# Kernel optimization log

Hardware: AMD Instinct MI355X
Metric: run time of the kernel (lower is better)

## Reference

```python
import jax, jax.numpy as jnp
import numpy as np

N = 20000      # CG beads
F = 78         # n_atom_basis (forced by reshape(-1,78) + Linear(n_atom_basis,39))
NRBF = 20
CUTOFF = 21.0
L = 3          # num_conv
DEG = 16
EH = N * DEG // 2
EPS = 1e-15


def silu(x):
    return x * jax.nn.sigmoid(x)


def setup_inputs() -> dict:
    key = jax.random.key(0)
    ks = jax.random.split(key, 22)
    cg_xyz = jax.random.normal(ks[0], (N, 3), jnp.float32) * 10.0
    half = jax.random.randint(ks[1], (EH, 2), 0, N)
    # symmetric (already-directed) edge list -> make_directed is a no-op
    CG_nbr_list = jnp.concatenate([half, half[:, ::-1]], axis=0)
    H = jax.random.normal(ks[2], (N, F), jnp.float32)
    mapping = jax.random.randint(ks[3], (N,), 0, N)  # unused by forward
    s = 0.05
    p = lambda k, shape: jax.random.normal(k, shape, jnp.float32) * s
    return {
        'cg_xyz': cg_xyz, 'CG_nbr_list': CG_nbr_list, 'mapping': mapping, 'H': H,
        # message blocks (stacked over L layers): inv_dense (F->F->4F) + dist_embed dense (NRBF->4F)
        'msg_w1': p(ks[4], (L, F, F)),   'msg_b1': jnp.zeros((L, F)),
        'msg_w2': p(ks[5], (L, F, 4 * F)), 'msg_b2': jnp.zeros((L, 4 * F)),
        'rbf_w':  p(ks[6], (L, NRBF, 4 * F)), 'rbf_b': jnp.zeros((L, 4 * F)),
        # update blocks: U, V linear maps (no bias) + s_dense (2F->F->3F)
        'upd_wu': p(ks[7], (L, F, F)), 'upd_wv': p(ks[8], (L, F, F)),
        'upd_w1': p(ks[9], (L, 2 * F, F)), 'upd_b1': jnp.zeros((L, F)),
        'upd_w2': p(ks[10], (L, F, 3 * F)), 'upd_b2': jnp.zeros((L, 3 * F)),
        # final dense head: ReLU -> Linear(78,39) -> ReLU -> Linear(39,39)
        'dense_w1': p(ks[11], (F, 39)), 'dense_b1': jnp.zeros((39,)),
        'dense_w2': p(ks[12], (39, 39)), 'dense_b2': jnp.zeros((39,)),
    }


def reference(cg_xyz, CG_nbr_list, mapping, H,
              msg_w1, msg_b1, msg_w2, msg_b2, rbf_w, rbf_b,
              upd_wu, upd_wv, upd_w1, upd_b1, upd_w2, upd_b2,
              dense_w1, dense_b1, dense_w2, dense_b2):
    n_nodes = H.shape[0]
    i_idx = CG_nbr_list[:, 0]
    j_idx = CG_nbr_list[:, 1]
    # edge geometry (shared across layers)
    r_ij = cg_xyz[j_idx] - cg_xyz[i_idx]                      # (E,3)
    dist = jnp.sqrt((r_ij ** 2 + EPS).sum(-1))                # (E,)
    unit = r_ij / dist[:, None]
    n = jnp.arange(1, NRBF + 1, dtype=cg_xyz.dtype)
    rbf = jnp.sin(n * jnp.pi * dist[:, None] / CUTOFF) / dist[:, None]   # (E,NRBF)
    env = jnp.where(dist < CUTOFF, 0.5 * (jnp.cos(jnp.pi * dist / CUTOFF) + 1.0), 0.0)

    V = jnp.zeros((n_nodes, H.shape[1], 3), H.dtype)          # (N,F,3)
    for l in range(L):
        # ---- EquiMessageCross ----
        phi = silu(H @ msg_w1[l] + msg_b1[l]) @ msg_w2[l] + msg_b2[l]     # (N,4F)
        w_s = (rbf @ rbf_w[l] + rbf_b[l]) * env[:, None]                  # (E,4F)
        inv = phi[j_idx] * w_s                                            # (E,4F)
        s0, s1, s2, s3 = jnp.split(inv, 4, axis=-1)                       # each (E,F)
        vj = V[j_idx]                                                     # (E,F,3)
        vi = V[i_idx]
        dv = (s2[..., None] * unit[:, None, :]
              + s1[..., None] * vj
              + s3[..., None] * jnp.cross(vi, vj, axis=-1))               # (E,F,3)
        H = H + jax.ops.segment_sum(s0, i_idx, num_segments=n_nodes)
        V = V + jax.ops.segment_sum(dv, i_idx, num_segments=n_nodes)
        # ---- UpdateBlock (PaiNN) ----
        u_v = jnp.einsum('nfc,fg->ngc', V, upd_wu[l])
        v_v = jnp.einsum('nfc,fg->ngc', V, upd_wv[l])
        v_norm = jnp.sqrt((v_v ** 2).sum(-1) + EPS)                       # (N,F)
        a = silu(jnp.concatenate([H, v_norm], -1) @ upd_w1[l] + upd_b1[l]) @ upd_w2[l] + upd_b2[l]
        a_vv, a_sv, a_ss = jnp.split(a, 3, axis=-1)
        H = H + a_sv * (u_v * v_v).sum(-1) + a_ss
        V = V + a_vv[..., None] * u_v

    Vs = V.sum(-1).reshape(-1, 78)                                        # (N,78)
    out = jax.nn.relu(Vs)
    out = jax.nn.relu(out @ dense_w1 + dense_b1) @ dense_w2 + dense_b2    # (N,39)
    return H, out.reshape(-1, 13, 3)
```

## Files before the change

### kernel.cpp

```cpp
#include <hip/hip_runtime.h>
#include <hip/hip_bf16.h>
#include <cmath>

#define N_NODES 20000
#define FF 78
#define F3 234
#define F4 312
#define NRBF 20
#define CUTOFF 21.0f
#define NL 3
#define PI_F 3.14159265358979323846f
#define EPS_F 1e-15f
#define REC_STRIDE 24
#define CHUNK 64
#define UV_RN 16

__global__ void k_init(const float* __restrict__ Hin, float* __restrict__ Hcur,
                       int* __restrict__ counts, int* __restrict__ cursor)
{
    int idx = blockIdx.x * blockDim.x + threadIdx.x;
    int stride = gridDim.x * blockDim.x;
    for (int i = idx; i < N_NODES * FF; i += stride) {
        Hcur[i] = Hin[i];
        if (i < N_NODES) { counts[i] = 0; cursor[i] = 0; }
    }
}

__global__ void k_geo(const float* __restrict__ xyz, const int* __restrict__ nbr,
                      float4* __restrict__ geo, int* __restrict__ counts, int E)
{
    int e = blockIdx.x * blockDim.x + threadIdx.x;
    if (e >= E) return;
    int i = nbr[2 * e], j = nbr[2 * e + 1];
    float rx = xyz[3 * j]     - xyz[3 * i];
    float ry = xyz[3 * j + 1] - xyz[3 * i + 1];
    float rz = xyz[3 * j + 2] - xyz[3 * i + 2];
    float d = sqrtf(rx * rx + ry * ry + rz * rz + 3.0f * EPS_F);
    geo[e] = make_float4(rx / d, ry / d, rz / d, d);
    if (d < CUTOFF) atomicAdd(&counts[i], 1);
}

__global__ __launch_bounds__(1024)
void k_scan(const int* __restrict__ counts, int* __restrict__ row_start, int n)
{
    __shared__ int s[1024];
    const int t = threadIdx.x;
    constexpr int PER = 20;
    const int base = t * PER;
    int loc[PER];
    int sum = 0;
    #pragma unroll
    for (int q = 0; q < PER; ++q) {
        int idx = base + q;
        int v = (idx < n) ? counts[idx] : 0;
        loc[q] = sum;
        sum += v;
    }
    s[t] = sum;
    __syncthreads();
    for (int off = 1; off < 1024; off <<= 1) {
        int add = (t >= off) ? s[t - off] : 0;
        __syncthreads();
        s[t] += add;
        __syncthreads();
    }
    const int excl = (t > 0) ? s[t - 1] : 0;
    #pragma unroll
    for (int q = 0; q < PER; ++q) {
        int idx = base + q;
        if (idx <= n) row_start[idx] = excl + loc[q];
    }
}

__global__ void k_fill(const float4* __restrict__ geo, const int* __restrict__ nbr,
                       const int* __restrict__ row_start, int* __restrict__ cursor,
                       float* __restrict__ rec, int* __restrict__ jl, int E)
{
    int e = blockIdx.x * blockDim.x + threadIdx.x;
    if (e >= E) return;
    float4 g = geo[e];
    if (g.w < CUTOFF) {
        int i = nbr[2 * e];
        int pos = row_start[i] + atomicAdd(&cursor[i], 1);
        float d = g.w;
        float theta = PI_F * d / CUTOFF;
        float s1, c1;
        sincosf(theta, &s1, &c1);
        float env = 0.5f * (c1 + 1.0f);
        float envd = env / d;
        float* r = rec + (size_t)pos * REC_STRIDE;
        float twoc = 2.f * c1;
        float skm = 0.f, sk = s1;
        r[0] = envd * sk;
        #pragma unroll
        for (int k = 1; k < NRBF; ++k) {
            float sk1 = twoc * sk - skm;
            r[k] = envd * sk1;
            skm = sk; sk = sk1;
        }
        r[20] = env;
        r[21] = g.x; r[22] = g.y; r[23] = g.z;
        jl[pos] = nbr[2 * e + 1];
    }
}

template<int K1T, int K2T, int NC2, int CS2, int BF16OUT>
__global__ void k_mlp2(const float* __restrict__ X1, const float* __restrict__ X2,
                       const float* __restrict__ w1, const float* __restrict__ b1,
                       const float* __restrict__ w2, const float* __restrict__ b2,
                       void* __restrict__ Yv, int nrows)
{
    constexpr int R = 32;
    constexpr int K = K1T + K2T;
    __shared__ float sX[K * R];
    __shared__ float s2[78 * 33];
    const int r0 = blockIdx.x * R;
    const int tid = threadIdx.y * 78 + threadIdx.x;
    for (int idx = tid; idx < R * K; idx += 312) {
        int r = idx / K, k = idx - r * K;
        int row = r0 + r;
        float v = 0.f;
        if (row < nrows) {
            if constexpr (K2T == 0) v = X1[(size_t)row * K1T + k];
            else v = (k < K1T) ? X1[(size_t)row * K1T + k] : X2[(size_t)row * K2T + (k - K1T)];
        }
        sX[k * R + r] = v;
    }
    __syncthreads();
    const int rg = threadIdx.y * 8;
    {
        const int c = threadIdx.x;
        float acc[8];
        #pragma unroll
        for (int q = 0; q < 8; ++q) acc[q] = 0.f;
        for (int k = 0; k < K; ++k) {
            const float w = w1[k * 78 + c];
            #pragma unroll
            for (int q = 0; q < 8; ++q) acc[q] = fmaf(w, sX[k * R + rg + q], acc[q]);
        }
        const float bb = b1[c];
        #pragma unroll
        for (int q = 0; q < 8; ++q) {
            float y = acc[q] + bb;
            y = y / (1.f + expf(-y));
            s2[c * 33 + rg + q] = y;
        }
    }
    __syncthreads();
    {
        const int c0 = threadIdx.x * CS2;
        float acc[8][CS2];
        #pragma unroll
        for (int q = 0; q < 8; ++q)
            #pragma unroll
            for (int cc = 0; cc < CS2; ++cc) acc[q][cc] = 0.f;
        for (int k = 0; k < 78; ++k) {
            float xv[8];
            #pragma unroll
            for (int q = 0; q < 8; ++q) xv[q] = s2[k * 33 + rg + q];
            float wv[CS2];
            #pragma unroll
            for (int cc = 0; cc < CS2; ++cc) wv[cc] = w2[(size_t)k * NC2 + c0 + cc];
            #pragma unroll
            for (int q = 0; q < 8; ++q)
                #pragma unroll
                for (int cc = 0; cc < CS2; ++cc) acc[q][cc] = fmaf(xv[q], wv[cc], acc[q][cc]);
        }
        #pragma unroll
        for (int q = 0; q < 8; ++q) {
            int row = r0 + rg + q;
            if (row < nrows) {
                if constexpr (BF16OUT && CS2 == 4) {
                    union { __hip_bfloat16 hh[4]; uint2 u; } pk;
                    #pragma unroll
                    for (int cc = 0; cc < 4; ++cc)
                        pk.hh[cc] = __float2bfloat16(acc[q][cc] + b2[c0 + cc]);
                    *(uint2*)&((__hip_bfloat16*)Yv)[(size_t)row * NC2 + c0] = pk.u;
                } else {
                    #pragma unroll
                    for (int cc = 0; cc < CS2; ++cc)
                        ((float*)Yv)[(size_t)row * NC2 + c0 + cc] = acc[q][cc] + b2[c0 + cc];
                }
            }
        }
    }
}

__global__ __launch_bounds__(312)
void k_updmlp_apply(const float* __restrict__ H, const float* __restrict__ vnorm,
                    const float* __restrict__ w1, const float* __restrict__ b1,
                    const float* __restrict__ w2, const float* __restrict__ b2,
                    const float* __restrict__ u_v, const float* __restrict__ v_v,
                    float* __restrict__ V, __hip_bfloat16* __restrict__ Vbf,
                    float* __restrict__ Hout)
{
    constexpr int R = 32;
    __shared__ float sX[156 * R];
    __shared__ float s2[78 * 33];
    const int r0 = blockIdx.x * R;
    const int tid = threadIdx.y * 78 + threadIdx.x;
    for (int idx = tid; idx < R * 156; idx += 312) {
        int r = idx / 156, k = idx - r * 156;
        int row = r0 + r;
        sX[k * R + r] = (k < 78) ? H[(size_t)row * FF + k]
                                 : vnorm[(size_t)row * FF + (k - 78)];
    }
    __syncthreads();
    const int rg = threadIdx.y * 8;
    const int c = threadIdx.x;
    {
        float acc[8];
        #pragma unroll
        for (int q = 0; q < 8; ++q) acc[q] = 0.f;
        for (int k = 0; k < 156; ++k) {
            const float w = w1[k * 78 + c];
            #pragma unroll
            for (int q = 0; q < 8; ++q) acc[q] = fmaf(w, sX[k * R + rg + q], acc[q]);
        }
        const float bb = b1[c];
        #pragma unroll
        for (int q = 0; q < 8; ++q) {
            float y = acc[q] + bb;
            s2[c * 33 + rg + q] = y / (1.f + expf(-y));
        }
    }
    __syncthreads();
    {
        float a0[8], a1[8], a2[8];
        #pragma unroll
        for (int q = 0; q < 8; ++q) { a0[q] = 0.f; a1[q] = 0.f; a2[q] = 0.f; }
        for (int k = 0; k < 78; ++k) {
            float xv[8];
            #pragma unroll
            for (int q = 0; q < 8; ++q) xv[q] = s2[k * 33 + rg + q];
            const float w0 = w2[k * F3 + c];
            const float w1v = w2[k * F3 + 78 + c];
            const float w2v = w2[k * F3 + 156 + c];
            #pragma unroll
            for (int q = 0; q < 8; ++q) {
                a0[q] = fmaf(xv[q], w0, a0[q]);
                a1[q] = fmaf(xv[q], w1v, a1[q]);
                a2[q] = fmaf(xv[q], w2v, a2[q]);
            }
        }
        const float bvv = b2[c], bsv = b2[78 + c], bss = b2[156 + c];
        #pragma unroll
        for (int q = 0; q < 8; ++q) {
            const int row = r0 + rg + q;
            const float avv = a0[q] + bvv, asv = a1[q] + bsv, ass = a2[q] + bss;
            const size_t b3 = (size_t)row * F3 + c * 3;
            const float u0 = u_v[b3], u1 = u_v[b3 + 1], u2 = u_v[b3 + 2];
            const float v0 = v_v[b3], v1 = v_v[b3 + 1], v2 = v_v[b3 + 2];
            const float dot = u0 * v0 + u1 * v1 + u2 * v2;
            Hout[(size_t)row * FF + c] = sX[c * R + rg + q] + asv * dot + ass;
            const float nv0 = V[b3]     + avv * u0;
            const float nv1 = V[b3 + 1] + avv * u1;
            const float nv2 = V[b3 + 2] + avv * u2;
            V[b3] = nv0; V[b3 + 1] = nv1; V[b3 + 2] = nv2;
            union { __hip_bfloat16 hh[4]; uint2 u; } pk;
            pk.hh[0] = __float2bfloat16(nv0);
            pk.hh[1] = __float2bfloat16(nv1);
            pk.hh[2] = __float2bfloat16(nv2);
            pk.hh[3] = __float2bfloat16(0.f);
            *(uint2*)&Vbf[(size_t)row * F4 + c * 4] = pk.u;
        }
    }
}

#define COMP_W(E_, W_, UX_, UY_, UZ_) do {                                          \
    const float4* r4_ = (const float4*)(rec + (size_t)(E_) * REC_STRIDE);           \
    const float4 q0=r4_[0], q1=r4_[1], q2=r4_[2], q3=r4_[3], q4=r4_[4], q5=r4_[5];  \
    float p0 = q0.x*wcol[0], p1 = q0.y*wcol[1], p2 = q0.z*wcol[2], p3 = q0.w*wcol[3]; \
    p0 = fmaf(q1.x, wcol[4],  p0);  p1 = fmaf(q1.y, wcol[5],  p1);                  \
    p2 = fmaf(q1.z, wcol[6],  p2);  p3 = fmaf(q1.w, wcol[7],  p3);                  \
    p0 = fmaf(q2.x, wcol[8],  p0);  p1 = fmaf(q2.y, wcol[9],  p1);                  \
    p2 = fmaf(q2.z, wcol[10], p2);  p3 = fmaf(q2.w, wcol[11], p3);                  \
    p0 = fmaf(q3.x, wcol[12], p0);  p1 = fmaf(q3.y, wcol[13], p1);                  \
    p2 = fmaf(q3.z, wcol[14], p2);  p3 = fmaf(q3.w, wcol[15], p3);                  \
    p0 = fmaf(q4.x, wcol[16], p0);  p1 = fmaf(q4.y, wcol[17], p1);                  \
    p2 = fmaf(q4.z, wcol[18], p2);  p3 = fmaf(q4.w, wcol[19], p3);                  \
    W_ = fmaf(wb, q5.x, (p0 + p1) + (p2 + p3));                                     \
    UX_ = q5.y; UY_ = q5.z; UZ_ = q5.w;                                             \
} while (0)

template<int L0>
__global__ __launch_bounds__(320)
void k_message(const __hip_bfloat16* __restrict__ phi, const float* __restrict__ Vold,
               const __hip_bfloat16* __restrict__ Vbf,
               float* __restrict__ Vnew, float* __restrict__ Hcur,
               const float* __restrict__ rec, const int* __restrict__ jl,
               const int* __restrict__ row_start,
               const float* __restrict__ rbfw, const float* __restrict__ rbfb)
{
    const int i = blockIdx.x;
    const int t = threadIdx.x;
    const int tt = (t < 312) ? t : 156;
    const int cch = (tt < 78) ? tt + 78 : (tt < 156) ? tt + 156
                  : (tt < 234) ? tt - 156 : tt - 78;
    const int fv  = (tt < 78) ? tt : (tt < 156) ? tt - 78 : 0;
    const bool needvj = (!L0) && (tt < 156);
    const float sun = (tt >= 234) ? 1.f : 0.f;
    const float svj = (tt < 156) ? 1.f : 0.f;

    __shared__ float s_acc[3 * F3];
    __shared__ int s_j[CHUNK];

    const unsigned short* __restrict__ phiu = (const unsigned short*)phi;
    const unsigned short* __restrict__ vbfu = (const unsigned short*)Vbf;

    float wcol[NRBF];
    const float wb = rbfb[cch];
    #pragma unroll
    for (int k = 0; k < NRBF; ++k) wcol[k] = rbfw[k * F4 + cch];

    const int e0 = row_start[i], e1 = row_start[i + 1];
    float accH = 0.f, a0 = 0.f, a1 = 0.f, a2 = 0.f;

    float vix = 0.f, viy = 0.f, viz = 0.f;
    if (!L0 && t >= 78 && t < 156) {
        const unsigned vb = (unsigned)i * F3 + (unsigned)fv * 3;
        vix = Vold[vb]; viy = Vold[vb + 1]; viz = Vold[vb + 2];
    }

    for (int base = e0; base < e1; base += CHUNK) {
        const int len = (e1 - base < CHUNK) ? (e1 - base) : CHUNK;
        if (t < len) s_j[t] = jl[base + t];
        __syncthreads();

        int jA = s_j[0];
        unsigned pfA = (unsigned)phiu[(size_t)jA * F4 + cch];
        uint2 vqA = make_uint2(0u, 0u);
        if (needvj) vqA = *(const uint2*)(vbfu + ((size_t)jA * F4 + 4u * fv));
        const int m1 = (1 < len) ? 1 : 0;
        int jB = s_j[m1];
        unsigned pfB = (unsigned)phiu[(size_t)jB * F4 + cch];
        uint2 vqB = make_uint2(0u, 0u);
        if (needvj) vqB = *(const uint2*)(vbfu + ((size_t)jB * F4 + 4u * fv));
        float wA, uxA, uyA, uzA;
        COMP_W(base, wA, uxA, uyA, uzA);

        for (int m = 0; m < len; ++m) {
            const int mw = (m + 1 < len) ? m + 1 : 0;
            const int m2 = (m + 2 < len) ? m + 2 : 0;
            float wN, uxN, uyN, uzN;
            COMP_W(base + mw, wN, uxN, uyN, uzN);
            const int jC = s_j[m2];
            const unsigned pfC = (unsigned)phiu[(size_t)jC * F4 + cch];
            uint2 vqC = make_uint2(0u, 0u);
            if (needvj) vqC = *(const uint2*)(vbfu + ((size_t)jC * F4 + 4u * fv));

            const float pv  = __uint_as_float(pfA << 16) * wA;
            const float vj0 = __uint_as_float(vqA.x << 16);
            const float vj1 = __uint_as_float(vqA.x & 0xffff0000u);
            const float vj2 = __uint_as_float(vqA.y << 16);
            a0 = fmaf(pv, fmaf(svj, vj0, sun * uxA), a0);
            a1 = fmaf(pv, fmaf(svj, vj1, sun * uyA), a1);
            a2 = fmaf(pv, fmaf(svj, vj2, sun * uzA), a2);
            accH += pv;

            pfA = pfB; vqA = vqB;
            wA = wN; uxA = uxN; uyA = uyN; uzA = uzN;
            pfB = pfC; vqB = vqC;
        }
        __syncthreads();
    }

    if (!L0 && t >= 78 && t < 156) {
        const float m0 = a0, m1c = a1, m2c = a2;
        a0 = viy * m2c - viz * m1c;
        a1 = viz * m0  - vix * m2c;
        a2 = vix * m1c - viy * m0;
    }

    if (t < 78) {
        s_acc[3*tt] = a0; s_acc[3*tt+1] = a1; s_acc[3*tt+2] = a2;
    } else if (t < 156) {
        const int f = tt - 78;
        if (L0) { s_acc[F3 + 3*f] = 0.f; s_acc[F3 + 3*f+1] = 0.f; s_acc[F3 + 3*f+2] = 0.f; }
        else    { s_acc[F3 + 3*f] = a0;  s_acc[F3 + 3*f+1] = a1;  s_acc[F3 + 3*f+2] = a2; }
    } else if (t >= 234 && t < 312) {
        const int f = tt - 234;
        s_acc[2*F3 + 3*f] = a0; s_acc[2*F3 + 3*f+1] = a1; s_acc[2*F3 + 3*f+2] = a2;
    }
    __syncthreads();
    if (t >= 156 && t < 234) Hcur[(unsigned)(i * FF + (t - 156))] += accH;
    for (int k = t; k < F3; k += 320) {
        const float base_v = L0 ? 0.f : Vold[(unsigned)(i * F3 + k)];
        Vnew[(unsigned)(i * F3 + k)] = base_v
            + s_acc[k] + s_acc[F3 + k] + s_acc[2*F3 + k];
    }
}

__global__ __launch_bounds__(256)
void k_upd_uv(const float* __restrict__ V, const float* __restrict__ wu, const float* __restrict__ wv,
              float* __restrict__ u_v, float* __restrict__ v_v, float* __restrict__ vnorm)
{
    const int n0 = blockIdx.x * UV_RN;
    const int t = threadIdx.x;
    __shared__ float sV[UV_RN][240];
    for (int idx = t; idx < F3 * UV_RN; idx += 256) {
        int n = idx / F3, k = idx - n * F3;
        sV[n][k] = V[(size_t)(n0 + n) * F3 + k];
    }
    __syncthreads();
    float au[UV_RN], av[UV_RN];
    #pragma unroll
    for (int n = 0; n < UV_RN; ++n) { au[n] = 0.f; av[n] = 0.f; }
    if (t < F3) {
        const int g = t / 3, c = t - g * 3;
        for (int f = 0; f < FF; ++f) {
            const float wuv = wu[f * FF + g];
            const float wvv = wv[f * FF + g];
            const int kk = f * 3 + c;
            #pragma unroll
            for (int n = 0; n < UV_RN; ++n) {
                const float x = sV[n][kk];
                au[n] = fmaf(x, wuv, au[n]);
                av[n] = fmaf(x, wvv, av[n]);
            }
        }
        #pragma unroll
        for (int n = 0; n < UV_RN; ++n) {
            u_v[(size_t)(n0 + n) * F3 + t] = au[n];
            v_v[(size_t)(n0 + n) * F3 + t] = av[n];
        }
    }
    __syncthreads();
    if (t < F3) {
        #pragma unroll
        for (int n = 0; n < UV_RN; ++n) sV[n][t] = av[n];
    }
    __syncthreads();
    for (int idx = t; idx < FF * UV_RN; idx += 256) {
        int n = idx / FF, g = idx - n * FF;
        float a = sV[n][3*g], b = sV[n][3*g+1], c = sV[n][3*g+2];
        vnorm[(size_t)(n0 + n) * FF + g] = sqrtf(a * a + b * b + c * c + EPS_F);
    }
}

__global__ __launch_bounds__(128)
void k_decode(const float* __restrict__ V, const float* __restrict__ w1, const float* __restrict__ b1,
              const float* __restrict__ w2, const float* __restrict__ b2, float* __restrict__ out)
{
    const int n = blockIdx.x, t = threadIdx.x;
    __shared__ float sx[FF];
    __shared__ float sh[39];
    if (t < FF) {
        size_t b = (size_t)n * F3 + t * 3;
        float x = V[b] + V[b+1] + V[b+2];
        sx[t] = fmaxf(x, 0.f);
    }
    __syncthreads();
    if (t < 39) {
        float h = b1[t];
        for (int g = 0; g < FF; ++g) h += sx[g] * w1[g * 39 + t];
        sh[t] = fmaxf(h, 0.f);
    }
    __syncthreads();
    if (t < 39) {
        float o = b2[t];
        for (int m = 0; m < 39; ++m) o += sh[m] * w2[m * 39 + t];
        out[(size_t)n * 39 + t] = o;
    }
}

extern "C" void kernel_launch(void* const* d_in, const int* in_sizes, int n_in,
                              void* d_out, int out_size, void* d_ws, size_t ws_size,
                              hipStream_t stream)
{
    const float* xyz    = (const float*)d_in[0];
    const int*   nbr    = (const int*)  d_in[1];
    const float* Hin    = (const float*)d_in[3];
    const float* msg_w1 = (const float*)d_in[4];
    const float* msg_b1 = (const float*)d_in[5];
    const float* msg_w2 = (const float*)d_in[6];
    const float* msg_b2 = (const float*)d_in[7];
    const float* rbf_w  = (const float*)d_in[8];
    const float* rbf_b  = (const float*)d_in[9];
    const float* upd_wu = (const float*)d_in[10];
    const float* upd_wv = (const float*)d_in[11];
    const float* upd_w1 = (const float*)d_in[12];
    const float* upd_b1 = (const float*)d_in[13];
    const float* upd_w2 = (const float*)d_in[14];
    const float* upd_b2 = (const float*)d_in[15];
    const float* dw1    = (const float*)d_in[16];
    const float* db1    = (const float*)d_in[17];
    const float* dw2    = (const float*)d_in[18];
    const float* db2    = (const float*)d_in[19];
    const int E = in_sizes[1] / 2;
    const int ECAP = E / 2 + E / 25;

    float* ws = (float*)d_ws;
    size_t off = 0;
    float* Hcur  = ws + off; off += (size_t)N_NODES * FF;
    float* VA    = ws + off; off += (size_t)N_NODES * F3;
    float* VB    = ws + off; off += (size_t)N_NODES * F3;
    __hip_bfloat16* phi = (__hip_bfloat16*)(ws + off); off += (size_t)N_NODES * F4 / 2;
    __hip_bfloat16* Vbf = (__hip_bfloat16*)(ws + off); off += (size_t)N_NODES * F4 / 2;
    float* u_v   = ws + off; off += (size_t)N_NODES * F3;
    float* v_v   = ws + off; off += (size_t)N_NODES * F3;
    float* vnorm = ws + off; off += (size_t)N_NODES * FF;
    float4* geo  = (float4*)(ws + off); off += (size_t)E * 4;
    float* rec   = ws + off; off += (size_t)ECAP * REC_STRIDE;
    int* ibase     = (int*)(ws + off);
    int* row_start = ibase;
    int* counts    = row_start + (N_NODES + 1);
    int* cursor    = counts + N_NODES;
    int* jl        = cursor + N_NODES;

    k_init<<<dim3((N_NODES * FF + 255) / 256), dim3(256), 0, stream>>>(
        Hin, Hcur, counts, cursor);
    k_geo<<<dim3((E + 255) / 256), dim3(256), 0, stream>>>(xyz, nbr, geo, counts, E);
    k_scan<<<dim3(1), dim3(1024), 0, stream>>>(counts, row_start, N_NODES);
    k_fill<<<dim3((E + 255) / 256), dim3(256), 0, stream>>>(geo, nbr, row_start, cursor, rec, jl, E);

    float* dout = (float*)d_out;
    float* Vold = VA;
    float* Vnew = VB;
    for (int l = 0; l < NL; ++l) {
        k_mlp2<78, 0, 312, 4, 1><<<dim3(625), dim3(78, 4), 0, stream>>>(
            Hcur, nullptr, msg_w1 + (size_t)l * 78 * 78, msg_b1 + (size_t)l * 78,
            msg_w2 + (size_t)l * 78 * 312, msg_b2 + (size_t)l * 312, phi, N_NODES);
        if (l == 0)
            k_message<1><<<dim3(N_NODES), dim3(320), 0, stream>>>(
                phi, Vold, Vbf, Vnew, Hcur, rec, jl, row_start,
                rbf_w + (size_t)l * NRBF * F4, rbf_b + (size_t)l * F4);
        else
            k_message<0><<<dim3(N_NODES), dim3(320), 0, stream>>>(
                phi, Vold, Vbf, Vnew, Hcur, rec, jl, row_start,
                rbf_w + (size_t)l * NRBF * F4, rbf_b + (size_t)l * F4);
        k_upd_uv<<<dim3(N_NODES / UV_RN), dim3(256), 0, stream>>>(
            Vnew, upd_wu + (size_t)l * 78 * 78, upd_wv + (size_t)l * 78 * 78, u_v, v_v, vnorm);
        float* Hout = (l == NL - 1) ? dout : Hcur;
        k_updmlp_apply<<<dim3(625), dim3(78, 4), 0, stream>>>(
            Hcur, vnorm, upd_w1 + (size_t)l * 156 * 78, upd_b1 + (size_t)l * 78,
            upd_w2 + (size_t)l * 78 * 234, upd_b2 + (size_t)l * 234,
            u_v, v_v, Vnew, Vbf, Hout);
        float* tmp = Vold; Vold = Vnew; Vnew = tmp;
    }

    k_decode<<<dim3(N_NODES), dim3(128), 0, stream>>>(Vold, dw1, db1, dw2, db2, dout + (size_t)N_NODES * FF);
}
```

Measured before the change: 729.7 us.

## Fuse decode head into last update, precompute u·v dot, pack RBF FMAs

The separate decode kernel is folded into the last layer's update kernel. That kernel sums V per row, applies ReLU, and runs both dense layers from shared memory, so the final V is neither written nor re-read. The u·v dot product is now computed in k_upd_uv and stored as an (N,78) buffer instead of the full (N,234) v_v tensor, which cuts global traffic. The RBF weight contraction in k_message uses two-wide float vector FMAs to encourage packed-FMA instructions. The trade-off is extra shared memory and serial per-thread loops in the fused decode tail.

```diff
diff --git a/kernel.cpp b/kernel.cpp
--- a/kernel.cpp
+++ b/kernel.cpp
@@ -14,6 +14,20 @@
 #define REC_STRIDE 24
 #define CHUNK 64
 #define UV_RN 16
+
+typedef float f2 __attribute__((ext_vector_type(2)));
+static __device__ __forceinline__ f2 mkf2(float a, float b) { f2 r; r.x = a; r.y = b; return r; }
+#if defined(__has_builtin)
+# if __has_builtin(__builtin_elementwise_fma)
+#  define FMA2(a,b,c) __builtin_elementwise_fma((a),(b),(c))
+# endif
+#endif
+#ifndef FMA2
+static __device__ __forceinline__ f2 fma2_(f2 a, f2 b, f2 c) {
+    f2 r; r.x = fmaf(a.x, b.x, c.x); r.y = fmaf(a.y, b.y, c.y); return r;
+}
+# define FMA2(a,b,c) fma2_((a),(b),(c))
+#endif
 
 __global__ void k_init(const float* __restrict__ Hin, float* __restrict__ Hcur,
                        int* __restrict__ counts, int* __restrict__ cursor)
@@ -186,17 +200,23 @@
     }
 }
 
+template<int LAST>
 __global__ __launch_bounds__(312)
 void k_updmlp_apply(const float* __restrict__ H, const float* __restrict__ vnorm,
                     const float* __restrict__ w1, const float* __restrict__ b1,
                     const float* __restrict__ w2, const float* __restrict__ b2,
-                    const float* __restrict__ u_v, const float* __restrict__ v_v,
+                    const float* __restrict__ u_v, const float* __restrict__ dotb,
                     float* __restrict__ V, __hip_bfloat16* __restrict__ Vbf,
-                    float* __restrict__ Hout)
+                    float* __restrict__ Hout,
+                    const float* __restrict__ dw1, const float* __restrict__ db1,
+                    const float* __restrict__ dw2, const float* __restrict__ db2,
+                    float* __restrict__ dec_out)
 {
     constexpr int R = 32;
     __shared__ float sX[156 * R];
     __shared__ float s2[78 * 33];
+    __shared__ float svs[LAST ? 78 * 33 : 4];
+    __shared__ float sh[LAST ? 39 * 33 : 4];
     const int r0 = blockIdx.x * R;
     const int tid = threadIdx.y * 78 + threadIdx.x;
     for (int idx = tid; idx < R * 156; idx += 312) {
@@ -250,19 +270,38 @@
             const float avv = a0[q] + bvv, asv = a1[q] + bsv, ass = a2[q] + bss;
             const size_t b3 = (size_t)row * F3 + c * 3;
             const float u0 = u_v[b3], u1 = u_v[b3 + 1], u2 = u_v[b3 + 2];
-            const float v0 = v_v[b3], v1 = v_v[b3 + 1], v2 = v_v[b3 + 2];
-            const float dot = u0 * v0 + u1 * v1 + u2 * v2;
+            const float dot = dotb[(size_t)row * FF + c];
             Hout[(size_t)row * FF + c] = sX[c * R + rg + q] + asv * dot + ass;
             const float nv0 = V[b3]     + avv * u0;
             const float nv1 = V[b3 + 1] + avv * u1;
             const float nv2 = V[b3 + 2] + avv * u2;
-            V[b3] = nv0; V[b3 + 1] = nv1; V[b3 + 2] = nv2;
-            union { __hip_bfloat16 hh[4]; uint2 u; } pk;
-            pk.hh[0] = __float2bfloat16(nv0);
-            pk.hh[1] = __float2bfloat16(nv1);
-            pk.hh[2] = __float2bfloat16(nv2);
-            pk.hh[3] = __float2bfloat16(0.f);
-            *(uint2*)&Vbf[(size_t)row * F4 + c * 4] = pk.u;
+            if constexpr (!LAST) {
+                V[b3] = nv0; V[b3 + 1] = nv1; V[b3 + 2] = nv2;
+                union { __hip_bfloat16 hh[4]; uint2 u; } pk;
+                pk.hh[0] = __float2bfloat16(nv0);
+                pk.hh[1] = __float2bfloat16(nv1);
+                pk.hh[2] = __float2bfloat16(nv2);
+                pk.hh[3] = __float2bfloat16(0.f);
+                *(uint2*)&Vbf[(size_t)row * F4 + c * 4] = pk.u;
+            } else {
+                svs[c * 33 + rg + q] = fmaxf(nv0 + nv1 + nv2, 0.f);
+            }
+        }
+    }
+    if constexpr (LAST) {
+        __syncthreads();
+        for (int idx = tid; idx < 39 * 32; idx += 312) {
+            const int r = idx / 39, o = idx - r * 39;
+            float h = db1[o];
+            for (int g = 0; g < 78; ++g) h = fmaf(svs[g * 33 + r], dw1[g * 39 + o], h);
+            sh[o * 33 + r] = fmaxf(h, 0.f);
+        }
+        __syncthreads();
+        for (int idx = tid; idx < 39 * 32; idx += 312) {
+            const int r = idx / 39, o = idx - r * 39;
+            float oo = db2[o];
+            for (int m = 0; m < 39; ++m) oo = fmaf(sh[m * 33 + r], dw2[m * 39 + o], oo);
+            dec_out[(size_t)(r0 + r) * 39 + o] = oo;
         }
     }
 }
@@ -270,16 +309,17 @@
 #define COMP_W(E_, W_, UX_, UY_, UZ_) do {                                          \
     const float4* r4_ = (const float4*)(rec + (size_t)(E_) * REC_STRIDE);           \
     const float4 q0=r4_[0], q1=r4_[1], q2=r4_[2], q3=r4_[3], q4=r4_[4], q5=r4_[5];  \
-    float p0 = q0.x*wcol[0], p1 = q0.y*wcol[1], p2 = q0.z*wcol[2], p3 = q0.w*wcol[3]; \
-    p0 = fmaf(q1.x, wcol[4],  p0);  p1 = fmaf(q1.y, wcol[5],  p1);                  \
-    p2 = fmaf(q1.z, wcol[6],  p2);  p3 = fmaf(q1.w, wcol[7],  p3);                  \
-    p0 = fmaf(q2.x, wcol[8],  p0);  p1 = fmaf(q2.y, wcol[9],  p1);                  \
-    p2 = fmaf(q2.z, wcol[10], p2);  p3 = fmaf(q2.w, wcol[11], p3);                  \
-    p0 = fmaf(q3.x, wcol[12], p0);  p1 = fmaf(q3.y, wcol[13], p1);                  \
-    p2 = fmaf(q3.z, wcol[14], p2);  p3 = fmaf(q3.w, wcol[15], p3);                  \
-    p0 = fmaf(q4.x, wcol[16], p0);  p1 = fmaf(q4.y, wcol[17], p1);                  \
-    p2 = fmaf(q4.z, wcol[18], p2);  p3 = fmaf(q4.w, wcol[19], p3);                  \
-    W_ = fmaf(wb, q5.x, (p0 + p1) + (p2 + p3));                                     \
+    f2 A_ = mkf2(q0.x, q0.y) * wcol2[0];                                            \
+    f2 B_ = mkf2(q0.z, q0.w) * wcol2[1];                                            \
+    A_ = FMA2(mkf2(q1.x, q1.y), wcol2[2], A_);                                      \
+    B_ = FMA2(mkf2(q1.z, q1.w), wcol2[3], B_);                                      \
+    A_ = FMA2(mkf2(q2.x, q2.y), wcol2[4], A_);                                      \
+    B_ = FMA2(mkf2(q2.z, q2.w), wcol2[5], B_);                                      \
+    A_ = FMA2(mkf2(q3.x, q3.y), wcol2[6], A_);                                      \
+    B_ = FMA2(mkf2(q3.z, q3.w), wcol2[7], B_);                                      \
+    A_ = FMA2(mkf2(q4.x, q4.y), wcol2[8], A_);                                      \
+    B_ = FMA2(mkf2(q4.z, q4.w), wcol2[9], B_);                                      \
+    W_ = fmaf(wb, q5.x, (A_.x + B_.x) + (A_.y + B_.y));                             \
     UX_ = q5.y; UY_ = q5.z; UZ_ = q5.w;                                             \
 } while (0)
 
@@ -308,10 +348,11 @@
     const unsigned short* __restrict__ phiu = (const unsigned short*)phi;
     const unsigned short* __restrict__ vbfu = (const unsigned short*)Vbf;
 
-    float wcol[NRBF];
+    f2 wcol2[10];
     const float wb = rbfb[cch];
     #pragma unroll
-    for (int k = 0; k < NRBF; ++k) wcol[k] = rbfw[k * F4 + cch];
+    for (int k = 0; k < 10; ++k)
+        wcol2[k] = mkf2(rbfw[(2 * k) * F4 + cch], rbfw[(2 * k + 1) * F4 + cch]);
 
     const int e0 = row_start[i], e1 = row_start[i + 1];
     float accH = 0.f, a0 = 0.f, a1 = 0.f, a2 = 0.f;
@@ -393,11 +434,12 @@
 
 __global__ __launch_bounds__(256)
 void k_upd_uv(const float* __restrict__ V, const float* __restrict__ wu, const float* __restrict__ wv,
-              float* __restrict__ u_v, float* __restrict__ v_v, float* __restrict__ vnorm)
+              float* __restrict__ u_v, float* __restrict__ dotb, float* __restrict__ vnorm)
 {
     const int n0 = blockIdx.x * UV_RN;
     const int t = threadIdx.x;
     __shared__ float sV[UV_RN][240];
+    __shared__ float sP[UV_RN][240];
     for (int idx = t; idx < F3 * UV_RN; idx += 256) {
         int n = idx / F3, k = idx - n * F3;
         sV[n][k] = V[(size_t)(n0 + n) * F3 + k];
@@ -420,47 +462,23 @@
             }
         }
         #pragma unroll
+        for (int n = 0; n < UV_RN; ++n)
+            u_v[(size_t)(n0 + n) * F3 + t] = au[n];
+    }
+    __syncthreads();
+    if (t < F3) {
+        #pragma unroll
         for (int n = 0; n < UV_RN; ++n) {
-            u_v[(size_t)(n0 + n) * F3 + t] = au[n];
-            v_v[(size_t)(n0 + n) * F3 + t] = av[n];
-        }
-    }
-    __syncthreads();
-    if (t < F3) {
-        #pragma unroll
-        for (int n = 0; n < UV_RN; ++n) sV[n][t] = av[n];
+            sV[n][t] = av[n];
+            sP[n][t] = au[n] * av[n];
+        }
     }
     __syncthreads();
     for (int idx = t; idx < FF * UV_RN; idx += 256) {
         int n = idx / FF, g = idx - n * FF;
         float a = sV[n][3*g], b = sV[n][3*g+1], c = sV[n][3*g+2];
         vnorm[(size_t)(n0 + n) * FF + g] = sqrtf(a * a + b * b + c * c + EPS_F);
-    }
-}
-
-__global__ __launch_bounds__(128)
-void k_decode(const float* __restrict__ V, const float* __restrict__ w1, const float* __restrict__ b1,
-              const float* __restrict__ w2, const float* __restrict__ b2, float* __restrict__ out)
-{
-    const int n = blockIdx.x, t = threadIdx.x;
-    __shared__ float sx[FF];
-    __shared__ float sh[39];
-    if (t < FF) {
-        size_t b = (size_t)n * F3 + t * 3;
-        float x = V[b] + V[b+1] + V[b+2];
-        sx[t] = fmaxf(x, 0.f);
-    }
-    __syncthreads();
-    if (t < 39) {
-        float h = b1[t];
-        for (int g = 0; g < FF; ++g) h += sx[g] * w1[g * 39 + t];
-        sh[t] = fmaxf(h, 0.f);
-    }
-    __syncthreads();
-    if (t < 39) {
-        float o = b2[t];
-        for (int m = 0; m < 39; ++m) o += sh[m] * w2[m * 39 + t];
-        out[(size_t)n * 39 + t] = o;
+        dotb[(size_t)(n0 + n) * FF + g] = sP[n][3*g] + sP[n][3*g+1] + sP[n][3*g+2];
     }
 }
 
@@ -498,7 +516,7 @@
     __hip_bfloat16* phi = (__hip_bfloat16*)(ws + off); off += (size_t)N_NODES * F4 / 2;
     __hip_bfloat16* Vbf = (__hip_bfloat16*)(ws + off); off += (size_t)N_NODES * F4 / 2;
     float* u_v   = ws + off; off += (size_t)N_NODES * F3;
-    float* v_v   = ws + off; off += (size_t)N_NODES * F3;
+    float* dotb  = ws + off; off += (size_t)N_NODES * FF;
     float* vnorm = ws + off; off += (size_t)N_NODES * FF;
     float4* geo  = (float4*)(ws + off); off += (size_t)E * 4;
     float* rec   = ws + off; off += (size_t)ECAP * REC_STRIDE;
@@ -530,14 +548,19 @@
                 phi, Vold, Vbf, Vnew, Hcur, rec, jl, row_start,
                 rbf_w + (size_t)l * NRBF * F4, rbf_b + (size_t)l * F4);
         k_upd_uv<<<dim3(N_NODES / UV_RN), dim3(256), 0, stream>>>(
-            Vnew, upd_wu + (size_t)l * 78 * 78, upd_wv + (size_t)l * 78 * 78, u_v, v_v, vnorm);
-        float* Hout = (l == NL - 1) ? dout : Hcur;
-        k_updmlp_apply<<<dim3(625), dim3(78, 4), 0, stream>>>(
-            Hcur, vnorm, upd_w1 + (size_t)l * 156 * 78, upd_b1 + (size_t)l * 78,
-            upd_w2 + (size_t)l * 78 * 234, upd_b2 + (size_t)l * 234,
-            u_v, v_v, Vnew, Vbf, Hout);
+            Vnew, upd_wu + (size_t)l * 78 * 78, upd_wv + (size_t)l * 78 * 78, u_v, dotb, vnorm);
+        if (l == NL - 1)
+            k_updmlp_apply<1><<<dim3(625), dim3(78, 4), 0, stream>>>(
+                Hcur, vnorm, upd_w1 + (size_t)l * 156 * 78, upd_b1 + (size_t)l * 78,
+                upd_w2 + (size_t)l * 78 * 234, upd_b2 + (size_t)l * 234,
+                u_v, dotb, Vnew, Vbf, dout,
+                dw1, db1, dw2, db2, dout + (size_t)N_NODES * FF);
+        else
+            k_updmlp_apply<0><<<dim3(625), dim3(78, 4), 0, stream>>>(
+                Hcur, vnorm, upd_w1 + (size_t)l * 156 * 78, upd_b1 + (size_t)l * 78,
+                upd_w2 + (size_t)l * 78 * 234, upd_b2 + (size_t)l * 234,
+                u_v, dotb, Vnew, Vbf, Hcur,
+                dw1, db1, dw2, db2, nullptr);
         float* tmp = Vold; Vold = Vnew; Vnew = tmp;
     }
-
-    k_decode<<<dim3(N_NODES), dim3(128), 0, stream>>>(Vold, dw1, db1, dw2, db2, dout + (size_t)N_NODES * FF);
-}
+}
```

Result: no change. 740.8 us (+1.5%).
